# Kernel optimization log

Measured on AMD Instinct MI355X. Metric: run time of the kernel, lower is better.

## Reference

```python
import jax, jax.numpy as jnp
import numpy as np

B, S, D = 2, 2048, 1024
H, KV, HD = 16, 4, 64          # query heads, kv heads, head_dim
ROT = 32                        # partial rotary dim
G = H // KV                     # GQA group size
SCALE = HD ** -0.5


def _rotate_half(x):
    x1, x2 = x[..., : x.shape[-1] // 2], x[..., x.shape[-1] // 2 :]
    return jnp.concatenate((-x2, x1), axis=-1)


def setup_inputs() -> dict:
    key = jax.random.key(0)
    ks = jax.random.split(key, 8)
    hidden_states = jax.random.normal(ks[0], (B, S, D), dtype=jnp.float32)
    # real rotary tables: inv_freq over ROT//2 frequencies, duplicated halves
    inv_freq = 1.0 / (10000.0 ** (jnp.arange(0, ROT, 2, dtype=jnp.float32) / ROT))
    ang = jnp.arange(S, dtype=jnp.float32)[:, None] * inv_freq[None, :]  # [S, ROT/2]
    emb = jnp.concatenate([ang, ang], axis=-1)                           # [S, ROT]
    cos = jnp.broadcast_to(jnp.cos(emb)[None], (B, S, ROT))
    sin = jnp.broadcast_to(jnp.sin(emb)[None], (B, S, ROT))
    sd = lambda fan_in: 1.0 / np.sqrt(fan_in)
    q_w = jax.random.normal(ks[1], (D, H * HD), jnp.float32) * sd(D)
    q_b = jax.random.normal(ks[2], (H * HD,), jnp.float32) * 0.02
    k_w = jax.random.normal(ks[3], (D, KV * HD), jnp.float32) * sd(D)
    v_w = jax.random.normal(ks[4], (D, KV * HD), jnp.float32) * sd(D)
    v_b = jax.random.normal(ks[5], (KV * HD,), jnp.float32) * 0.02
    o_w = jax.random.normal(ks[6], (H * HD, D), jnp.float32) * sd(H * HD)
    o_b = jax.random.normal(ks[7], (D,), jnp.float32) * 0.02
    return {"hidden_states": hidden_states, "cos": cos, "sin": sin,
            "q_w": q_w, "q_b": q_b, "k_w": k_w, "v_w": v_w, "v_b": v_b,
            "o_w": o_w, "o_b": o_b}


def reference(hidden_states, cos, sin, q_w, q_b, k_w, v_w, v_b, o_w, o_b):
    x = hidden_states
    # projections -> [B, heads, S, HD]
    q = (x @ q_w + q_b).reshape(B, S, H, HD).transpose(0, 2, 1, 3)
    k = (x @ k_w).reshape(B, S, KV, HD).transpose(0, 2, 1, 3)
    v = (x @ v_w + v_b).reshape(B, S, KV, HD).transpose(0, 2, 1, 3)
    # partial RoPE; cos/sin broadcast over head dim
    c = cos[:, None, :, :]
    s = sin[:, None, :, :]
    q_rot, q_pass = q[..., :ROT], q[..., ROT:]
    k_rot, k_pass = k[..., :ROT], k[..., ROT:]
    q = jnp.concatenate([q_rot * c + _rotate_half(q_rot) * s, q_pass], axis=-1)
    k = jnp.concatenate([k_rot * c + _rotate_half(k_rot) * s, k_pass], axis=-1)
    # GQA without materializing repeated K/V: group queries per kv head
    qg = q.reshape(B, KV, G, S, HD)
    scores = jnp.einsum("bkgsd,bktd->bkgst", qg, k) * SCALE  # [B,KV,G,S,S]
    probs = jax.nn.softmax(scores, axis=-1)
    out = jnp.einsum("bkgst,bktd->bkgsd", probs, v)          # [B,KV,G,S,HD]
    out = out.reshape(B, H, S, HD).transpose(0, 2, 1, 3).reshape(B, S, H * HD)
    attn_output = out @ o_w + o_b
    attn_weights = probs.reshape(B, H, S, S)
    return attn_output, attn_weights
```

## Files before the change

kernel.cpp:

```cpp
#include <hip/hip_runtime.h>
#include <hip/hip_bf16.h>

typedef _Float16 f16;
typedef _Float16 f16x8 __attribute__((ext_vector_type(8)));
typedef _Float16 f16x4 __attribute__((ext_vector_type(4)));
typedef float f32x4 __attribute__((ext_vector_type(4)));

#define MFMA_F16(a, b, c) __builtin_amdgcn_mfma_f32_16x16x32_f16((a), (b), (c), 0, 0, 0)

static constexpr int S_TOK = 2048;
static constexpr int N_HEAD = 16;
static constexpr int N_KV = 4;
static constexpr int HD = 64;
static constexpr float SCL2E = 0.125f * 1.4426950408889634f;

__global__ __launch_bounds__(256) void k_qkv(
    const float* __restrict__ x, const float* __restrict__ cosp,
    const float* __restrict__ sinp, const float* __restrict__ q_w,
    const float* __restrict__ q_b, const float* __restrict__ k_w,
    const float* __restrict__ v_w, const float* __restrict__ v_b,
    f16* __restrict__ q_ws, f16* __restrict__ k_ws, f16* __restrict__ v_ws) {
  __shared__ f16 wb[64][72];
  const int tid = threadIdx.x;
  const int wave = tid >> 6, lane = tid & 63;
  const int l16 = lane & 15, g = lane >> 4;
  const int m0 = blockIdx.x * 64;
  const int n0 = blockIdx.y * 64;

  const float* W;
  int ldW, nloc, mode;
  if (n0 < 1024) { W = q_w; ldW = 1024; nloc = n0; mode = 0; }
  else if (n0 < 1280) { W = k_w; ldW = 256; nloc = n0 - 1024; mode = 1; }
  else { W = v_w; ldW = 256; nloc = n0 - 1280; mode = 2; }

  f32x4 acc[4] = {};
  const int kk = (tid >> 4) * 4;
  const int nn = (tid & 15) * 4;

  for (int k0 = 0; k0 < 1024; k0 += 64) {
    const float* wp = W + (size_t)(k0 + kk) * ldW + nloc + nn;
    float4 w0 = *(const float4*)(wp);
    float4 w1 = *(const float4*)(wp + ldW);
    float4 w2 = *(const float4*)(wp + 2 * ldW);
    float4 w3 = *(const float4*)(wp + 3 * ldW);
    __syncthreads();
    *(f16x4*)&wb[nn + 0][kk] = f16x4{(f16)w0.x, (f16)w1.x, (f16)w2.x, (f16)w3.x};
    *(f16x4*)&wb[nn + 1][kk] = f16x4{(f16)w0.y, (f16)w1.y, (f16)w2.y, (f16)w3.y};
    *(f16x4*)&wb[nn + 2][kk] = f16x4{(f16)w0.z, (f16)w1.z, (f16)w2.z, (f16)w3.z};
    *(f16x4*)&wb[nn + 3][kk] = f16x4{(f16)w0.w, (f16)w1.w, (f16)w2.w, (f16)w3.w};
    __syncthreads();
    const float* xp = x + (size_t)(m0 + wave * 16 + l16) * 1024 + k0 + g * 8;
#pragma unroll
    for (int ks = 0; ks < 2; ++ks) {
      float4 a0 = *(const float4*)(xp + ks * 32);
      float4 a1 = *(const float4*)(xp + ks * 32 + 4);
      f16x8 af = {(f16)a0.x, (f16)a0.y, (f16)a0.z, (f16)a0.w,
                  (f16)a1.x, (f16)a1.y, (f16)a1.z, (f16)a1.w};
#pragma unroll
      for (int n = 0; n < 4; ++n) {
        f16x8 bf = *(const f16x8*)&wb[n * 16 + l16][ks * 32 + g * 8];
        acc[n] = MFMA_F16(af, bf, acc[n]);
      }
    }
  }

  if (mode == 0) {
#pragma unroll
    for (int n = 0; n < 4; ++n) {
      float bsc = q_b[n0 + n * 16 + l16];
#pragma unroll
      for (int r = 0; r < 4; ++r) acc[n][r] += bsc;
    }
  } else if (mode == 2) {
#pragma unroll
    for (int n = 0; n < 4; ++n) {
      float bsc = v_b[nloc + n * 16 + l16];
#pragma unroll
      for (int r = 0; r < 4; ++r) acc[n][r] += bsc;
    }
  }
  if (mode < 2) {
#pragma unroll
    for (int r = 0; r < 4; ++r) {
      int row = m0 + wave * 16 + g * 4 + r;
      int bb = row >> 11, ss = row & 2047;
      float c = cosp[((size_t)bb * S_TOK + ss) * 32 + l16];
      float sn = sinp[((size_t)bb * S_TOK + ss) * 32 + l16];
      float v0 = acc[0][r], v1 = acc[1][r];
      acc[0][r] = v0 * c - v1 * sn;
      acc[1][r] = v1 * c + v0 * sn;
    }
  }
#pragma unroll
  for (int n = 0; n < 4; ++n) {
#pragma unroll
    for (int r = 0; r < 4; ++r) {
      int row = m0 + wave * 16 + g * 4 + r;
      int bb = row >> 11, ss = row & 2047;
      f16 val = (f16)acc[n][r];
      if (mode == 0) {
        int col = n0 + n * 16 + l16;
        int h = col >> 6, hd = col & 63;
        q_ws[(((size_t)bb * N_HEAD + h) * S_TOK + ss) * HD + hd] = val;
      } else {
        int col = nloc + n * 16 + l16;
        int kh = col >> 6, hd = col & 63;
        if (mode == 1)
          k_ws[(((size_t)bb * N_KV + kh) * S_TOK + ss) * HD + hd] = val;
        else
          v_ws[(((size_t)bb * N_KV + kh) * HD + hd) * S_TOK + ss] = val;
      }
    }
  }
}

__global__ __launch_bounds__(256) void k_attn(
    const f16* __restrict__ q_ws, const f16* __restrict__ k_ws,
    const f16* __restrict__ v_ws, f16* __restrict__ o_ws,
    float* __restrict__ probs) {
  __shared__ f16 plds_all[4][32][72];
  const int tid = threadIdx.x;
  const int wave = tid >> 6, lane = tid & 63;
  const int l16 = lane & 15, g = lane >> 4;
  const int head = blockIdx.x >> 4;
  const int rt = blockIdx.x & 15;
  const int b = head >> 4, h = head & 15, kvh = h >> 2;
  const int qrow0 = rt * 128 + wave * 32;

  const f16* qb = q_ws + ((size_t)head * S_TOK + qrow0) * HD;
  const f16* kb = k_ws + (size_t)(b * N_KV + kvh) * S_TOK * HD;
  const f16* vb = v_ws + (size_t)(b * N_KV + kvh) * HD * S_TOK;
  float* pout = probs + (size_t)head * S_TOK * S_TOK + (size_t)qrow0 * S_TOK;
  f16(*plds)[72] = plds_all[wave];

  f16x8 qf[2][2];
#pragma unroll
  for (int mf = 0; mf < 2; ++mf)
#pragma unroll
    for (int ks = 0; ks < 2; ++ks)
      qf[mf][ks] = *(const f16x8*)(qb + (mf * 16 + l16) * HD + ks * 32 + g * 8);

  float lsum[2][4] = {};
  for (int kt = 0; kt < 32; ++kt) {
    const f16* kp = kb + (size_t)kt * 64 * HD;
    f16x8 kf[4][2];
#pragma unroll
    for (int n = 0; n < 4; ++n)
#pragma unroll
      for (int ks = 0; ks < 2; ++ks)
        kf[n][ks] = *(const f16x8*)(kp + (n * 16 + l16) * HD + ks * 32 + g * 8);
#pragma unroll
    for (int mf = 0; mf < 2; ++mf)
#pragma unroll
      for (int n = 0; n < 4; ++n) {
        f32x4 s = {};
        s = MFMA_F16(qf[mf][0], kf[n][0], s);
        s = MFMA_F16(qf[mf][1], kf[n][1], s);
#pragma unroll
        for (int r = 0; r < 4; ++r) lsum[mf][r] += exp2f(s[r] * SCL2E);
      }
  }
#pragma unroll
  for (int mf = 0; mf < 2; ++mf)
#pragma unroll
    for (int r = 0; r < 4; ++r) {
      float v = lsum[mf][r];
      v += __shfl_xor(v, 1, 64);
      v += __shfl_xor(v, 2, 64);
      v += __shfl_xor(v, 4, 64);
      v += __shfl_xor(v, 8, 64);
      lsum[mf][r] = 1.0f / v;
    }

  f32x4 oacc[2][4] = {};
  const int orow = lane >> 3, oq = lane & 7;
  for (int kt = 0; kt < 32; ++kt) {
    const f16* kp = kb + (size_t)kt * 64 * HD;
    f16x8 kf[4][2];
#pragma unroll
    for (int n = 0; n < 4; ++n)
#pragma unroll
      for (int ks = 0; ks < 2; ++ks)
        kf[n][ks] = *(const f16x8*)(kp + (n * 16 + l16) * HD + ks * 32 + g * 8);
#pragma unroll
    for (int mf = 0; mf < 2; ++mf)
#pragma unroll
      for (int n = 0; n < 4; ++n) {
        f32x4 s = {};
        s = MFMA_F16(qf[mf][0], kf[n][0], s);
        s = MFMA_F16(qf[mf][1], kf[n][1], s);
#pragma unroll
        for (int r = 0; r < 4; ++r) {
          float p = exp2f(s[r] * SCL2E) * lsum[mf][r];
          plds[mf * 16 + g * 4 + r][n * 16 + l16] = (f16)p;
        }
      }
    asm volatile("s_waitcnt lgkmcnt(0)" ::: "memory");
    f16x8 pa[2][2];
#pragma unroll
    for (int mf = 0; mf < 2; ++mf)
#pragma unroll
      for (int ks = 0; ks < 2; ++ks)
        pa[mf][ks] = *(const f16x8*)&plds[mf * 16 + l16][ks * 32 + g * 8];
    f16x8 vf[4][2];
#pragma unroll
    for (int nh = 0; nh < 4; ++nh)
#pragma unroll
      for (int ks = 0; ks < 2; ++ks)
        vf[nh][ks] = *(const f16x8*)(vb + (size_t)(nh * 16 + l16) * S_TOK +
                                     kt * 64 + ks * 32 + g * 8);
#pragma unroll
    for (int mf = 0; mf < 2; ++mf)
#pragma unroll
      for (int nh = 0; nh < 4; ++nh) {
        oacc[mf][nh] = MFMA_F16(pa[mf][0], vf[nh][0], oacc[mf][nh]);
        oacc[mf][nh] = MFMA_F16(pa[mf][1], vf[nh][1], oacc[mf][nh]);
      }
#pragma unroll
    for (int it = 0; it < 4; ++it) {
      int rr = it * 8 + orow;
      f16x8 pv = *(const f16x8*)&plds[rr][oq * 8];
      f32x4 lo = {(float)pv[0], (float)pv[1], (float)pv[2], (float)pv[3]};
      f32x4 hi = {(float)pv[4], (float)pv[5], (float)pv[6], (float)pv[7]};
      float* dst = pout + (size_t)rr * S_TOK + kt * 64 + oq * 8;
      *(f32x4*)dst = lo;
      *(f32x4*)(dst + 4) = hi;
    }
    asm volatile("" ::: "memory");
  }
#pragma unroll
  for (int mf = 0; mf < 2; ++mf)
#pragma unroll
    for (int nh = 0; nh < 4; ++nh)
#pragma unroll
      for (int r = 0; r < 4; ++r) {
        int srow = qrow0 + mf * 16 + g * 4 + r;
        o_ws[((size_t)b * S_TOK + srow) * 1024 + h * HD + nh * 16 + l16] =
            (f16)oacc[mf][nh][r];
      }
}

__global__ __launch_bounds__(256) void k_oproj(
    const f16* __restrict__ a, const float* __restrict__ o_w,
    const float* __restrict__ o_b, float* __restrict__ out) {
  __shared__ f16 wb[64][72];
  const int tid = threadIdx.x;
  const int wave = tid >> 6, lane = tid & 63;
  const int l16 = lane & 15, g = lane >> 4;
  const int m0 = blockIdx.x * 64, n0 = blockIdx.y * 64;
  f32x4 acc[4] = {};
  const int kk = (tid >> 4) * 4, nn = (tid & 15) * 4;
  for (int k0 = 0; k0 < 1024; k0 += 64) {
    const float* wp = o_w + (size_t)(k0 + kk) * 1024 + n0 + nn;
    float4 w0 = *(const float4*)(wp);
    float4 w1 = *(const float4*)(wp + 1024);
    float4 w2 = *(const float4*)(wp + 2048);
    float4 w3 = *(const float4*)(wp + 3072);
    __syncthreads();
    *(f16x4*)&wb[nn + 0][kk] = f16x4{(f16)w0.x, (f16)w1.x, (f16)w2.x, (f16)w3.x};
    *(f16x4*)&wb[nn + 1][kk] = f16x4{(f16)w0.y, (f16)w1.y, (f16)w2.y, (f16)w3.y};
    *(f16x4*)&wb[nn + 2][kk] = f16x4{(f16)w0.z, (f16)w1.z, (f16)w2.z, (f16)w3.z};
    *(f16x4*)&wb[nn + 3][kk] = f16x4{(f16)w0.w, (f16)w1.w, (f16)w2.w, (f16)w3.w};
    __syncthreads();
    const f16* ap = a + (size_t)(m0 + wave * 16 + l16) * 1024 + k0 + g * 8;
#pragma unroll
    for (int ks = 0; ks < 2; ++ks) {
      f16x8 af = *(const f16x8*)(ap + ks * 32);
#pragma unroll
      for (int n = 0; n < 4; ++n) {
        f16x8 bf = *(const f16x8*)&wb[n * 16 + l16][ks * 32 + g * 8];
        acc[n] = MFMA_F16(af, bf, acc[n]);
      }
    }
  }
#pragma unroll
  for (int n = 0; n < 4; ++n) {
    float bsc = o_b[n0 + n * 16 + l16];
#pragma unroll
    for (int r = 0; r < 4; ++r) {
      int row = m0 + wave * 16 + g * 4 + r;
      out[(size_t)row * 1024 + n0 + n * 16 + l16] = acc[n][r] + bsc;
    }
  }
}

extern "C" void kernel_launch(void* const* d_in, const int* in_sizes, int n_in,
                              void* d_out, int out_size, void* d_ws,
                              size_t ws_size, hipStream_t stream) {
  (void)in_sizes; (void)n_in; (void)out_size; (void)ws_size;
  const float* x    = (const float*)d_in[0];
  const float* cosp = (const float*)d_in[1];
  const float* sinp = (const float*)d_in[2];
  const float* q_w  = (const float*)d_in[3];
  const float* q_b  = (const float*)d_in[4];
  const float* k_w  = (const float*)d_in[5];
  const float* v_w  = (const float*)d_in[6];
  const float* v_b  = (const float*)d_in[7];
  const float* o_w  = (const float*)d_in[8];
  const float* o_b  = (const float*)d_in[9];

  f16* q_ws = (f16*)d_ws;
  f16* k_ws = q_ws + 4194304;
  f16* v_ws = k_ws + 1048576;
  f16* o_ws = v_ws + 1048576;
  float* out = (float*)d_out;
  float* probs = out + 4194304;

  k_qkv<<<dim3(64, 24), 256, 0, stream>>>(x, cosp, sinp, q_w, q_b, k_w, v_w,
                                          v_b, q_ws, k_ws, v_ws);
  k_attn<<<dim3(512), 256, 0, stream>>>(q_ws, k_ws, v_ws, o_ws, probs);
  k_oproj<<<dim3(64, 16), 256, 0, stream>>>(o_ws, o_w, o_b, out);
}
```

Baseline: 344.5 us.

## Pre-convert inputs to f16 and split attention KV range across wave pairs

Adds a conversion kernel that casts x and all weights to f16 once, so the projection GEMMs load half the bytes and skip per-tile conversion. The attention kernel now splits each query tile's key range between two waves, combining softmax denominators and partial outputs through shared memory. This doubles the grid and adds a launch-bounds occupancy hint. Probabilities are written with narrower nontemporal stores. The cost is an extra kernel launch and extra shared-memory syncs in exchange for more parallelism on the probs-write-bound attention.

```diff
diff --git a/kernel.cpp b/kernel.cpp
--- a/kernel.cpp
+++ b/kernel.cpp
@@ -14,11 +14,39 @@
 static constexpr int HD = 64;
 static constexpr float SCL2E = 0.125f * 1.4426950408889634f;
 
+static constexpr size_t OFF_X16 = 0;
+static constexpr size_t OFF_QW = 4194304;
+static constexpr size_t OFF_KW = OFF_QW + 1048576;
+static constexpr size_t OFF_VW = OFF_KW + 262144;
+static constexpr size_t OFF_OW = OFF_VW + 262144;
+static constexpr size_t OFF_QS = OFF_OW + 1048576;
+static constexpr size_t OFF_KS = OFF_QS + 4194304;
+static constexpr size_t OFF_VS = OFF_KS + 1048576;
+static constexpr size_t OFF_OS = OFF_VS + 1048576;
+static constexpr size_t CVT_TOTAL = OFF_OW + 1048576;
+
+__global__ __launch_bounds__(256) void k_cvt(
+    const float* __restrict__ x, const float* __restrict__ qw,
+    const float* __restrict__ kw, const float* __restrict__ vw,
+    const float* __restrict__ ow, f16* __restrict__ dst) {
+  size_t i = ((size_t)blockIdx.x * 256 + threadIdx.x) * 4;
+  if (i >= CVT_TOTAL) return;
+  const float* src;
+  size_t off;
+  if (i < OFF_QW) { src = x; off = i; }
+  else if (i < OFF_KW) { src = qw; off = i - OFF_QW; }
+  else if (i < OFF_VW) { src = kw; off = i - OFF_KW; }
+  else if (i < OFF_OW) { src = vw; off = i - OFF_VW; }
+  else { src = ow; off = i - OFF_OW; }
+  float4 v = *(const float4*)(src + off);
+  *(f16x4*)(dst + i) = f16x4{(f16)v.x, (f16)v.y, (f16)v.z, (f16)v.w};
+}
+
 __global__ __launch_bounds__(256) void k_qkv(
-    const float* __restrict__ x, const float* __restrict__ cosp,
-    const float* __restrict__ sinp, const float* __restrict__ q_w,
-    const float* __restrict__ q_b, const float* __restrict__ k_w,
-    const float* __restrict__ v_w, const float* __restrict__ v_b,
+    const f16* __restrict__ x, const float* __restrict__ cosp,
+    const float* __restrict__ sinp, const f16* __restrict__ q_w,
+    const float* __restrict__ q_b, const f16* __restrict__ k_w,
+    const f16* __restrict__ v_w, const float* __restrict__ v_b,
     f16* __restrict__ q_ws, f16* __restrict__ k_ws, f16* __restrict__ v_ws) {
   __shared__ f16 wb[64][72];
   const int tid = threadIdx.x;
@@ -27,7 +55,7 @@
   const int m0 = blockIdx.x * 64;
   const int n0 = blockIdx.y * 64;
 
-  const float* W;
+  const f16* W;
   int ldW, nloc, mode;
   if (n0 < 1024) { W = q_w; ldW = 1024; nloc = n0; mode = 0; }
   else if (n0 < 1280) { W = k_w; ldW = 256; nloc = n0 - 1024; mode = 1; }
@@ -38,24 +66,21 @@
   const int nn = (tid & 15) * 4;
 
   for (int k0 = 0; k0 < 1024; k0 += 64) {
-    const float* wp = W + (size_t)(k0 + kk) * ldW + nloc + nn;
-    float4 w0 = *(const float4*)(wp);
-    float4 w1 = *(const float4*)(wp + ldW);
-    float4 w2 = *(const float4*)(wp + 2 * ldW);
-    float4 w3 = *(const float4*)(wp + 3 * ldW);
+    const f16* wp = W + (size_t)(k0 + kk) * ldW + nloc + nn;
+    f16x4 w0 = *(const f16x4*)(wp);
+    f16x4 w1 = *(const f16x4*)(wp + ldW);
+    f16x4 w2 = *(const f16x4*)(wp + 2 * ldW);
+    f16x4 w3 = *(const f16x4*)(wp + 3 * ldW);
     __syncthreads();
-    *(f16x4*)&wb[nn + 0][kk] = f16x4{(f16)w0.x, (f16)w1.x, (f16)w2.x, (f16)w3.x};
-    *(f16x4*)&wb[nn + 1][kk] = f16x4{(f16)w0.y, (f16)w1.y, (f16)w2.y, (f16)w3.y};
-    *(f16x4*)&wb[nn + 2][kk] = f16x4{(f16)w0.z, (f16)w1.z, (f16)w2.z, (f16)w3.z};
-    *(f16x4*)&wb[nn + 3][kk] = f16x4{(f16)w0.w, (f16)w1.w, (f16)w2.w, (f16)w3.w};
+    *(f16x4*)&wb[nn + 0][kk] = f16x4{w0[0], w1[0], w2[0], w3[0]};
+    *(f16x4*)&wb[nn + 1][kk] = f16x4{w0[1], w1[1], w2[1], w3[1]};
+    *(f16x4*)&wb[nn + 2][kk] = f16x4{w0[2], w1[2], w2[2], w3[2]};
+    *(f16x4*)&wb[nn + 3][kk] = f16x4{w0[3], w1[3], w2[3], w3[3]};
     __syncthreads();
-    const float* xp = x + (size_t)(m0 + wave * 16 + l16) * 1024 + k0 + g * 8;
+    const f16* xp = x + (size_t)(m0 + wave * 16 + l16) * 1024 + k0 + g * 8;
 #pragma unroll
     for (int ks = 0; ks < 2; ++ks) {
-      float4 a0 = *(const float4*)(xp + ks * 32);
-      float4 a1 = *(const float4*)(xp + ks * 32 + 4);
-      f16x8 af = {(f16)a0.x, (f16)a0.y, (f16)a0.z, (f16)a0.w,
-                  (f16)a1.x, (f16)a1.y, (f16)a1.z, (f16)a1.w};
+      f16x8 af = *(const f16x8*)(xp + ks * 32);
 #pragma unroll
       for (int n = 0; n < 4; ++n) {
         f16x8 bf = *(const f16x8*)&wb[n * 16 + l16][ks * 32 + g * 8];
@@ -114,18 +139,21 @@
   }
 }
 
-__global__ __launch_bounds__(256) void k_attn(
+__global__ __launch_bounds__(256, 3) void k_attn(
     const f16* __restrict__ q_ws, const f16* __restrict__ k_ws,
     const f16* __restrict__ v_ws, f16* __restrict__ o_ws,
     float* __restrict__ probs) {
   __shared__ f16 plds_all[4][32][72];
+  __shared__ float lpart[2][2][32];
+  __shared__ float osum[2][32][68];
   const int tid = threadIdx.x;
   const int wave = tid >> 6, lane = tid & 63;
+  const int pairi = wave >> 1, half = wave & 1;
   const int l16 = lane & 15, g = lane >> 4;
-  const int head = blockIdx.x >> 4;
-  const int rt = blockIdx.x & 15;
+  const int head = blockIdx.x >> 5;
+  const int rt = blockIdx.x & 31;
   const int b = head >> 4, h = head & 15, kvh = h >> 2;
-  const int qrow0 = rt * 128 + wave * 32;
+  const int qrow0 = rt * 64 + pairi * 32;
 
   const f16* qb = q_ws + ((size_t)head * S_TOK + qrow0) * HD;
   const f16* kb = k_ws + (size_t)(b * N_KV + kvh) * S_TOK * HD;
@@ -140,25 +168,24 @@
     for (int ks = 0; ks < 2; ++ks)
       qf[mf][ks] = *(const f16x8*)(qb + (mf * 16 + l16) * HD + ks * 32 + g * 8);
 
+  const int kt0 = half * 16, kt1 = kt0 + 16;
+
   float lsum[2][4] = {};
-  for (int kt = 0; kt < 32; ++kt) {
+  for (int kt = kt0; kt < kt1; ++kt) {
     const f16* kp = kb + (size_t)kt * 64 * HD;
-    f16x8 kf[4][2];
-#pragma unroll
-    for (int n = 0; n < 4; ++n)
-#pragma unroll
-      for (int ks = 0; ks < 2; ++ks)
-        kf[n][ks] = *(const f16x8*)(kp + (n * 16 + l16) * HD + ks * 32 + g * 8);
-#pragma unroll
-    for (int mf = 0; mf < 2; ++mf)
-#pragma unroll
-      for (int n = 0; n < 4; ++n) {
+#pragma unroll
+    for (int n = 0; n < 4; ++n) {
+      f16x8 k0f = *(const f16x8*)(kp + (n * 16 + l16) * HD + g * 8);
+      f16x8 k1f = *(const f16x8*)(kp + (n * 16 + l16) * HD + 32 + g * 8);
+#pragma unroll
+      for (int mf = 0; mf < 2; ++mf) {
         f32x4 s = {};
-        s = MFMA_F16(qf[mf][0], kf[n][0], s);
-        s = MFMA_F16(qf[mf][1], kf[n][1], s);
+        s = MFMA_F16(qf[mf][0], k0f, s);
+        s = MFMA_F16(qf[mf][1], k1f, s);
 #pragma unroll
         for (int r = 0; r < 4; ++r) lsum[mf][r] += exp2f(s[r] * SCL2E);
       }
+    }
   }
 #pragma unroll
   for (int mf = 0; mf < 2; ++mf)
@@ -169,32 +196,45 @@
       v += __shfl_xor(v, 2, 64);
       v += __shfl_xor(v, 4, 64);
       v += __shfl_xor(v, 8, 64);
-      lsum[mf][r] = 1.0f / v;
+      lsum[mf][r] = v;
+    }
+  if (l16 == 0) {
+#pragma unroll
+    for (int mf = 0; mf < 2; ++mf)
+#pragma unroll
+      for (int r = 0; r < 4; ++r)
+        lpart[pairi][half][mf * 16 + g * 4 + r] = lsum[mf][r];
+  }
+  __syncthreads();
+  float linv[2][4];
+#pragma unroll
+  for (int mf = 0; mf < 2; ++mf)
+#pragma unroll
+    for (int r = 0; r < 4; ++r) {
+      int row = mf * 16 + g * 4 + r;
+      linv[mf][r] = 1.0f / (lpart[pairi][0][row] + lpart[pairi][1][row]);
     }
 
   f32x4 oacc[2][4] = {};
-  const int orow = lane >> 3, oq = lane & 7;
-  for (int kt = 0; kt < 32; ++kt) {
+  const int orow = lane >> 4, oq = lane & 15;
+  for (int kt = kt0; kt < kt1; ++kt) {
     const f16* kp = kb + (size_t)kt * 64 * HD;
-    f16x8 kf[4][2];
-#pragma unroll
-    for (int n = 0; n < 4; ++n)
-#pragma unroll
-      for (int ks = 0; ks < 2; ++ks)
-        kf[n][ks] = *(const f16x8*)(kp + (n * 16 + l16) * HD + ks * 32 + g * 8);
-#pragma unroll
-    for (int mf = 0; mf < 2; ++mf)
-#pragma unroll
-      for (int n = 0; n < 4; ++n) {
+#pragma unroll
+    for (int n = 0; n < 4; ++n) {
+      f16x8 k0f = *(const f16x8*)(kp + (n * 16 + l16) * HD + g * 8);
+      f16x8 k1f = *(const f16x8*)(kp + (n * 16 + l16) * HD + 32 + g * 8);
+#pragma unroll
+      for (int mf = 0; mf < 2; ++mf) {
         f32x4 s = {};
-        s = MFMA_F16(qf[mf][0], kf[n][0], s);
-        s = MFMA_F16(qf[mf][1], kf[n][1], s);
+        s = MFMA_F16(qf[mf][0], k0f, s);
+        s = MFMA_F16(qf[mf][1], k1f, s);
 #pragma unroll
         for (int r = 0; r < 4; ++r) {
-          float p = exp2f(s[r] * SCL2E) * lsum[mf][r];
+          float p = exp2f(s[r] * SCL2E) * linv[mf][r];
           plds[mf * 16 + g * 4 + r][n * 16 + l16] = (f16)p;
         }
       }
+    }
     asm volatile("s_waitcnt lgkmcnt(0)" ::: "memory");
     f16x8 pa[2][2];
 #pragma unroll
@@ -202,46 +242,55 @@
 #pragma unroll
       for (int ks = 0; ks < 2; ++ks)
         pa[mf][ks] = *(const f16x8*)&plds[mf * 16 + l16][ks * 32 + g * 8];
-    f16x8 vf[4][2];
-#pragma unroll
-    for (int nh = 0; nh < 4; ++nh)
-#pragma unroll
-      for (int ks = 0; ks < 2; ++ks)
-        vf[nh][ks] = *(const f16x8*)(vb + (size_t)(nh * 16 + l16) * S_TOK +
-                                     kt * 64 + ks * 32 + g * 8);
+#pragma unroll
+    for (int nh = 0; nh < 4; ++nh) {
+      const f16* vp = vb + (size_t)(nh * 16 + l16) * S_TOK + kt * 64;
+      f16x8 v0f = *(const f16x8*)(vp + g * 8);
+      f16x8 v1f = *(const f16x8*)(vp + 32 + g * 8);
+#pragma unroll
+      for (int mf = 0; mf < 2; ++mf) {
+        oacc[mf][nh] = MFMA_F16(pa[mf][0], v0f, oacc[mf][nh]);
+        oacc[mf][nh] = MFMA_F16(pa[mf][1], v1f, oacc[mf][nh]);
+      }
+    }
+#pragma unroll
+    for (int it = 0; it < 8; ++it) {
+      int rr = it * 4 + orow;
+      f16x4 pv = *(const f16x4*)&plds[rr][oq * 4];
+      f32x4 ov = {(float)pv[0], (float)pv[1], (float)pv[2], (float)pv[3]};
+      __builtin_nontemporal_store(
+          ov, (f32x4*)(pout + (size_t)rr * S_TOK + kt * 64 + oq * 4));
+    }
+    asm volatile("" ::: "memory");
+  }
+
+  if (half == 1) {
 #pragma unroll
     for (int mf = 0; mf < 2; ++mf)
 #pragma unroll
-      for (int nh = 0; nh < 4; ++nh) {
-        oacc[mf][nh] = MFMA_F16(pa[mf][0], vf[nh][0], oacc[mf][nh]);
-        oacc[mf][nh] = MFMA_F16(pa[mf][1], vf[nh][1], oacc[mf][nh]);
-      }
-#pragma unroll
-    for (int it = 0; it < 4; ++it) {
-      int rr = it * 8 + orow;
-      f16x8 pv = *(const f16x8*)&plds[rr][oq * 8];
-      f32x4 lo = {(float)pv[0], (float)pv[1], (float)pv[2], (float)pv[3]};
-      f32x4 hi = {(float)pv[4], (float)pv[5], (float)pv[6], (float)pv[7]};
-      float* dst = pout + (size_t)rr * S_TOK + kt * 64 + oq * 8;
-      *(f32x4*)dst = lo;
-      *(f32x4*)(dst + 4) = hi;
-    }
-    asm volatile("" ::: "memory");
-  }
-#pragma unroll
-  for (int mf = 0; mf < 2; ++mf)
-#pragma unroll
-    for (int nh = 0; nh < 4; ++nh)
-#pragma unroll
-      for (int r = 0; r < 4; ++r) {
-        int srow = qrow0 + mf * 16 + g * 4 + r;
-        o_ws[((size_t)b * S_TOK + srow) * 1024 + h * HD + nh * 16 + l16] =
-            (f16)oacc[mf][nh][r];
-      }
+      for (int nh = 0; nh < 4; ++nh)
+#pragma unroll
+        for (int r = 0; r < 4; ++r)
+          osum[pairi][mf * 16 + g * 4 + r][nh * 16 + l16] = oacc[mf][nh][r];
+  }
+  __syncthreads();
+  if (half == 0) {
+#pragma unroll
+    for (int mf = 0; mf < 2; ++mf)
+#pragma unroll
+      for (int nh = 0; nh < 4; ++nh)
+#pragma unroll
+        for (int r = 0; r < 4; ++r) {
+          int row = mf * 16 + g * 4 + r;
+          float v = oacc[mf][nh][r] + osum[pairi][row][nh * 16 + l16];
+          o_ws[((size_t)b * S_TOK + qrow0 + row) * 1024 + h * HD + nh * 16 +
+               l16] = (f16)v;
+        }
+  }
 }
 
 __global__ __launch_bounds__(256) void k_oproj(
-    const f16* __restrict__ a, const float* __restrict__ o_w,
+    const f16* __restrict__ a, const f16* __restrict__ o_w,
     const float* __restrict__ o_b, float* __restrict__ out) {
   __shared__ f16 wb[64][72];
   const int tid = threadIdx.x;
@@ -251,16 +300,16 @@
   f32x4 acc[4] = {};
   const int kk = (tid >> 4) * 4, nn = (tid & 15) * 4;
   for (int k0 = 0; k0 < 1024; k0 += 64) {
-    const float* wp = o_w + (size_t)(k0 + kk) * 1024 + n0 + nn;
-    float4 w0 = *(const float4*)(wp);
-    float4 w1 = *(const float4*)(wp + 1024);
-    float4 w2 = *(const float4*)(wp + 2048);
-    float4 w3 = *(const float4*)(wp + 3072);
+    const f16* wp = o_w + (size_t)(k0 + kk) * 1024 + n0 + nn;
+    f16x4 w0 = *(const f16x4*)(wp);
+    f16x4 w1 = *(const f16x4*)(wp + 1024);
+    f16x4 w2 = *(const f16x4*)(wp + 2048);
+    f16x4 w3 = *(const f16x4*)(wp + 3072);
     __syncthreads();
-    *(f16x4*)&wb[nn + 0][kk] = f16x4{(f16)w0.x, (f16)w1.x, (f16)w2.x, (f16)w3.x};
-    *(f16x4*)&wb[nn + 1][kk] = f16x4{(f16)w0.y, (f16)w1.y, (f16)w2.y, (f16)w3.y};
-    *(f16x4*)&wb[nn + 2][kk] = f16x4{(f16)w0.z, (f16)w1.z, (f16)w2.z, (f16)w3.z};
-    *(f16x4*)&wb[nn + 3][kk] = f16x4{(f16)w0.w, (f16)w1.w, (f16)w2.w, (f16)w3.w};
+    *(f16x4*)&wb[nn + 0][kk] = f16x4{w0[0], w1[0], w2[0], w3[0]};
+    *(f16x4*)&wb[nn + 1][kk] = f16x4{w0[1], w1[1], w2[1], w3[1]};
+    *(f16x4*)&wb[nn + 2][kk] = f16x4{w0[2], w1[2], w2[2], w3[2]};
+    *(f16x4*)&wb[nn + 3][kk] = f16x4{w0[3], w1[3], w2[3], w3[3]};
     __syncthreads();
     const f16* ap = a + (size_t)(m0 + wave * 16 + l16) * 1024 + k0 + g * 8;
 #pragma unroll
@@ -299,15 +348,23 @@
   const float* o_w  = (const float*)d_in[8];
   const float* o_b  = (const float*)d_in[9];
 
-  f16* q_ws = (f16*)d_ws;
-  f16* k_ws = q_ws + 4194304;
-  f16* v_ws = k_ws + 1048576;
-  f16* o_ws = v_ws + 1048576;
+  f16* ws = (f16*)d_ws;
+  f16* x16  = ws + OFF_X16;
+  f16* qw16 = ws + OFF_QW;
+  f16* kw16 = ws + OFF_KW;
+  f16* vw16 = ws + OFF_VW;
+  f16* ow16 = ws + OFF_OW;
+  f16* q_ws = ws + OFF_QS;
+  f16* k_ws = ws + OFF_KS;
+  f16* v_ws = ws + OFF_VS;
+  f16* o_ws = ws + OFF_OS;
   float* out = (float*)d_out;
   float* probs = out + 4194304;
 
-  k_qkv<<<dim3(64, 24), 256, 0, stream>>>(x, cosp, sinp, q_w, q_b, k_w, v_w,
-                                          v_b, q_ws, k_ws, v_ws);
-  k_attn<<<dim3(512), 256, 0, stream>>>(q_ws, k_ws, v_ws, o_ws, probs);
-  k_oproj<<<dim3(64, 16), 256, 0, stream>>>(o_ws, o_w, o_b, out);
-}
+  k_cvt<<<dim3((CVT_TOTAL / 4 + 255) / 256), 256, 0, stream>>>(
+      x, q_w, k_w, v_w, o_w, ws);
+  k_qkv<<<dim3(64, 24), 256, 0, stream>>>(x16, cosp, sinp, qw16, q_b, kw16,
+                                          vw16, v_b, q_ws, k_ws, v_ws);
+  k_attn<<<dim3(1024), 256, 0, stream>>>(q_ws, k_ws, v_ws, o_ws, probs);
+  k_oproj<<<dim3(64, 16), 256, 0, stream>>>(o_ws, ow16, o_b, out);
+}
```

Result: faster. 298.1 us (-13.4%).
